# Kernel optimization log

Measured on AMD Instinct MI355X. Metric: run time of the kernel, lower is better.

Reference implementation:

```python
import jax, jax.numpy as jnp
import numpy as np


def setup_inputs() -> dict:
    key = jax.random.key(0)
    ks = jax.random.split(key, 6)
    B, S, D, U = 32, 2048, 1024, 1024
    scale = 1.0 / np.sqrt(D)
    return {
        "h_enc": jax.random.normal(ks[0], (B, S, D), dtype=jnp.float32),
        "h_dec": jax.random.normal(ks[1], (B, D), dtype=jnp.float32),
        "W_enc": jax.random.normal(ks[2], (D, U), dtype=jnp.float32) * scale,
        "b_enc": jnp.zeros((U,), dtype=jnp.float32),
        "W_dec": jax.random.normal(ks[3], (D, U), dtype=jnp.float32) * scale,
        "b_dec": jnp.zeros((U,), dtype=jnp.float32),
        "W_com": jax.random.normal(ks[4], (U, 1), dtype=jnp.float32) * (1.0 / np.sqrt(U)),
        "b_com": jnp.zeros((1,), dtype=jnp.float32),
    }


def reference(h_enc, h_dec, W_enc, b_enc, W_dec, b_dec, W_com, b_com):
    # h_enc: [B,S,D] -> projected enc features [B,S,U]
    enc_p = jnp.einsum("bsd,du->bsu", h_enc, W_enc) + b_enc
    # h_dec: [B,D] -> [B,1,U]
    dec_p = (h_dec @ W_dec + b_dec)[:, None, :]
    # additive score: [B,S,1]
    score = jnp.einsum("bsu,uo->bso", jnp.tanh(dec_p + enc_p), W_com) + b_com
    attn = jax.nn.softmax(score, axis=1)  # softmax over seq axis
    # NOTE: original code multiplies attn by the PROJECTED h_enc (reassigned)
    context_vec = jnp.sum(attn * enc_p, axis=1)  # [B,U]
    return (context_vec, attn)
```

## Files before the change

### kernel.cpp

```cpp
#include <hip/hip_runtime.h>
#include <math.h>
#include <stdint.h>

#define Bz 32
#define Sz 2048
#define Dz 1024
#define Uz 1024
#define Mz (Bz*Sz)

typedef __attribute__((ext_vector_type(8))) short bf16x8;
typedef __attribute__((ext_vector_type(4))) float f32x4;

__device__ __forceinline__ unsigned short f2bf(float f) {
    union { float f; uint32_t u; } v; v.f = f;
    uint32_t r = v.u + 0x7FFFu + ((v.u >> 16) & 1u);
    return (unsigned short)(r >> 16);
}

__device__ __forceinline__ float fast_tanh(float x) {
    float e = __expf(2.f * x);
    return 1.f - 2.f * __builtin_amdgcn_rcpf(e + 1.f);
}

#define GLD16(gsrc, ldst) \
    __builtin_amdgcn_global_load_lds((__attribute__((address_space(1))) void*)(void*)(gsrc), \
        (__attribute__((address_space(3))) void*)(ldst), 16, 0, 0)

#define CONV_BLOCKS 16384
#define WT_BLOCKS   256
#define DECI_BLOCKS 32
#define SINIT_BLOCKS 64

__global__ __launch_bounds__(256) void prep_kernel(
    const float* __restrict__ h_enc, unsigned short* __restrict__ hbf,
    const float* __restrict__ W_enc, unsigned short* __restrict__ wT,
    const float* __restrict__ b_dec, float* __restrict__ dec_p,
    const float* __restrict__ b_com, float* __restrict__ score)
{
    __shared__ float tile[64][65];
    const int bid = blockIdx.x;
    const int tid = threadIdx.x;
    if (bid < CONV_BLOCKS) {
        const size_t i = ((size_t)bid * 256 + tid) * 16;
#pragma unroll
        for (int h = 0; h < 2; ++h) {
            const float4 a = *(const float4*)(h_enc + i + h * 8);
            const float4 c = *(const float4*)(h_enc + i + h * 8 + 4);
            union { unsigned short s[8]; uint4 v; } o;
            o.s[0] = f2bf(a.x); o.s[1] = f2bf(a.y); o.s[2] = f2bf(a.z); o.s[3] = f2bf(a.w);
            o.s[4] = f2bf(c.x); o.s[5] = f2bf(c.y); o.s[6] = f2bf(c.z); o.s[7] = f2bf(c.w);
            *(uint4*)(hbf + i + h * 8) = o.v;
        }
    } else if (bid < CONV_BLOCKS + WT_BLOCKS) {
        const int b2 = bid - CONV_BLOCKS;
        const int c  = tid & 63;
        const int r0 = tid >> 6;
        const int u0 = (b2 & 15) * 64;
        const int d0 = (b2 >> 4) * 64;
        for (int r = r0; r < 64; r += 4)
            tile[r][c] = W_enc[(size_t)(d0 + r) * Uz + u0 + c];
        __syncthreads();
        for (int r = r0; r < 64; r += 4)
            wT[(size_t)(u0 + r) * Dz + d0 + c] = f2bf(tile[c][r]);
    } else if (bid < CONV_BLOCKS + WT_BLOCKS + DECI_BLOCKS) {
        const int b3 = bid - (CONV_BLOCKS + WT_BLOCKS);
        const int u4 = tid * 4;
        *(float4*)&dec_p[b3 * Uz + u4] = *(const float4*)&b_dec[u4];
    } else {
        const int b4 = bid - (CONV_BLOCKS + WT_BLOCKS + DECI_BLOCKS);
        const float bc = b_com[0];
        const int i4 = (b4 * 256 + tid) * 4;
        float4 v = {bc, bc, bc, bc};
        *(float4*)&score[i4] = v;
    }
}

__global__ __launch_bounds__(256) void dec_partial_kernel(
    const float* __restrict__ h_dec, const float* __restrict__ W_dec,
    float* __restrict__ dec_p)
{
    __shared__ float hs[128];
    const int b  = blockIdx.x >> 3;
    const int d0 = (blockIdx.x & 7) * 128;
    const int tid = threadIdx.x;
    const int u4 = tid * 4;
    if (tid < 128) hs[tid] = h_dec[b * Dz + d0 + tid];
    __syncthreads();
    float4 acc = {0.f, 0.f, 0.f, 0.f};
#pragma unroll 4
    for (int d = 0; d < 128; ++d) {
        const float  a = hs[d];
        const float4 w = *(const float4*)&W_dec[(size_t)(d0 + d) * Uz + u4];
        acc.x += a * w.x; acc.y += a * w.y; acc.z += a * w.z; acc.w += a * w.w;
    }
    float* o = dec_p + b * Uz + u4;
    atomicAdd(o + 0, acc.x); atomicAdd(o + 1, acc.y);
    atomicAdd(o + 2, acc.z); atomicAdd(o + 3, acc.w);
}

__global__ __launch_bounds__(256) void score_mfma_kernel(
    const unsigned short* __restrict__ hbf,
    const unsigned short* __restrict__ wT,
    const float* __restrict__ dec_p,
    const float* __restrict__ W_com,
    float* __restrict__ score)
{
    __shared__ unsigned short As[8 * 512];
    __shared__ unsigned short Bs[8 * 512];

    const int tid  = threadIdx.x;
    const int w    = tid >> 6;
    const int lane = tid & 63;
    const int ln   = lane & 15;
    const int q    = lane >> 4;
    const int wm   = w & 1;
    const int wn   = w >> 1;
    const int m0   = (blockIdx.x >> 1) * 128;
    const int uh   = blockIdx.x & 1;
    const int b    = m0 / Sz;
    const int ub   = uh * 512;

    const int g0 = 2 * w;
    const unsigned short* a_src0 = hbf + (size_t)(m0 + g0 * 16 + ln) * Dz + q * 8;
    const unsigned short* a_src1 = a_src0 + (size_t)16 * Dz;
    unsigned short* a_dst0 = As + g0 * 512;
    unsigned short* a_dst1 = a_dst0 + 512;

    float racc[4][4];
#pragma unroll
    for (int i = 0; i < 4; ++i)
#pragma unroll
        for (int r = 0; r < 4; ++r) racc[i][r] = 0.f;

    for (int u0 = 0; u0 < 512; u0 += 128) {
        f32x4 acc[4][4];
#pragma unroll
        for (int i = 0; i < 4; ++i)
#pragma unroll
            for (int j = 0; j < 4; ++j) acc[i][j] = (f32x4){0.f, 0.f, 0.f, 0.f};

        const unsigned short* b_src0 = wT + (size_t)(ub + u0 + g0 * 16 + ln) * Dz + q * 8;
        const unsigned short* b_src1 = b_src0 + (size_t)16 * Dz;
        unsigned short* b_dst0 = Bs + g0 * 512;
        unsigned short* b_dst1 = b_dst0 + 512;

        for (int k0 = 0; k0 < Dz; k0 += 32) {
            __syncthreads();
            GLD16(a_src0 + k0, a_dst0);
            GLD16(a_src1 + k0, a_dst1);
            GLD16(b_src0 + k0, b_dst0);
            GLD16(b_src1 + k0, b_dst1);
            __syncthreads();

            bf16x8 af[4], bfr[4];
#pragma unroll
            for (int i = 0; i < 4; ++i)
                af[i] = *(const bf16x8*)(As + (wm * 4 + i) * 512 + lane * 8);
#pragma unroll
            for (int j = 0; j < 4; ++j)
                bfr[j] = *(const bf16x8*)(Bs + (wn * 4 + j) * 512 + lane * 8);
#pragma unroll
            for (int i = 0; i < 4; ++i)
#pragma unroll
                for (int j = 0; j < 4; ++j)
                    acc[i][j] = __builtin_amdgcn_mfma_f32_16x16x32_bf16(
                        af[i], bfr[j], acc[i][j], 0, 0, 0);
        }

        float dpv[4], wcv[4];
#pragma unroll
        for (int j = 0; j < 4; ++j) {
            const int u = ub + u0 + (wn * 4 + j) * 16 + ln;
            dpv[j] = dec_p[b * Uz + u];
            wcv[j] = W_com[u];
        }
#pragma unroll
        for (int i = 0; i < 4; ++i)
#pragma unroll
            for (int r = 0; r < 4; ++r) {
                float v = 0.f;
#pragma unroll
                for (int j = 0; j < 4; ++j)
                    v += fast_tanh(acc[i][j][r] + dpv[j]) * wcv[j];
                racc[i][r] += v;
            }
    }

#pragma unroll
    for (int off = 1; off < 16; off <<= 1)
#pragma unroll
        for (int i = 0; i < 4; ++i)
#pragma unroll
            for (int r = 0; r < 4; ++r)
                racc[i][r] += __shfl_xor(racc[i][r], off, 64);
    if (ln == 0) {
#pragma unroll
        for (int i = 0; i < 4; ++i)
#pragma unroll
            for (int r = 0; r < 4; ++r)
                atomicAdd(&score[m0 + wm * 64 + i * 16 + q * 4 + r], racc[i][r]);
    }
}

__global__ __launch_bounds__(256) void softmax_init_kernel(
    const float* __restrict__ score, float* __restrict__ attn,
    const float* __restrict__ b_enc, float* __restrict__ out_ctx,
    float* __restrict__ wsum)
{
    __shared__ float red[256];
    const int tid = threadIdx.x;
    if (blockIdx.x >= 2 * Bz) {
        const int b3 = blockIdx.x - 2 * Bz;
        float4 z = {0.f, 0.f, 0.f, 0.f};
        *(float4*)&wsum[b3 * Dz + tid * 4] = z;
        return;
    }
    if (blockIdx.x >= Bz) {
        const int b2 = blockIdx.x - Bz;
        const int u4 = tid * 4;
        *(float4*)&out_ctx[b2 * Uz + u4] = *(const float4*)&b_enc[u4];
        return;
    }
    const int b = blockIdx.x;
    const float* srow = score + b * Sz;
    float v[8];
    float lm = -1e30f;
#pragma unroll
    for (int i = 0; i < 8; ++i) { v[i] = srow[i * 256 + tid]; lm = fmaxf(lm, v[i]); }
    red[tid] = lm; __syncthreads();
    for (int off = 128; off > 0; off >>= 1) {
        if (tid < off) red[tid] = fmaxf(red[tid], red[tid + off]);
        __syncthreads();
    }
    const float mx = red[0];
    __syncthreads();
    float ls = 0.f;
#pragma unroll
    for (int i = 0; i < 8; ++i) { v[i] = expf(v[i] - mx); ls += v[i]; }
    red[tid] = ls; __syncthreads();
    for (int off = 128; off > 0; off >>= 1) {
        if (tid < off) red[tid] += red[tid + off];
        __syncthreads();
    }
    const float inv = 1.f / red[0];
#pragma unroll
    for (int i = 0; i < 8; ++i) attn[b * Sz + i * 256 + tid] = v[i] * inv;
}

__global__ __launch_bounds__(256) void wsum_kernel(
    const float* __restrict__ h_enc, const float* __restrict__ attn,
    float* __restrict__ wsum)
{
    __shared__ float aw[64];
    const int b  = blockIdx.x >> 5;
    const int s0 = (blockIdx.x & 31) * 64;
    const int tid = threadIdx.x;
    if (tid < 64) aw[tid] = attn[b * Sz + s0 + tid];
    __syncthreads();
    float4 acc = {0.f, 0.f, 0.f, 0.f};
    const float* base = h_enc + ((size_t)b * Sz + s0) * Dz + tid * 4;
#pragma unroll 4
    for (int s = 0; s < 64; ++s) {
        const float a = aw[s];
        const float4 h = *(const float4*)(base + (size_t)s * Dz);
        acc.x += a * h.x; acc.y += a * h.y; acc.z += a * h.z; acc.w += a * h.w;
    }
    float* o = wsum + b * Dz + tid * 4;
    atomicAdd(o + 0, acc.x); atomicAdd(o + 1, acc.y);
    atomicAdd(o + 2, acc.z); atomicAdd(o + 3, acc.w);
}

__global__ __launch_bounds__(256) void ctx_partial_kernel(
    const float* __restrict__ wsum, const float* __restrict__ W_enc,
    float* __restrict__ out_ctx)
{
    __shared__ float hs[128];
    const int b  = blockIdx.x >> 3;
    const int d0 = (blockIdx.x & 7) * 128;
    const int tid = threadIdx.x;
    const int u4 = tid * 4;
    if (tid < 128) hs[tid] = wsum[b * Dz + d0 + tid];
    __syncthreads();
    float4 acc = {0.f, 0.f, 0.f, 0.f};
#pragma unroll 4
    for (int d = 0; d < 128; ++d) {
        const float  a = hs[d];
        const float4 wv = *(const float4*)&W_enc[(size_t)(d0 + d) * Uz + u4];
        acc.x += a * wv.x; acc.y += a * wv.y; acc.z += a * wv.z; acc.w += a * wv.w;
    }
    float* o = out_ctx + b * Uz + u4;
    atomicAdd(o + 0, acc.x); atomicAdd(o + 1, acc.y);
    atomicAdd(o + 2, acc.z); atomicAdd(o + 3, acc.w);
}

__global__ __launch_bounds__(256) void dec_proj_kernel(
    const float* __restrict__ h_dec, const float* __restrict__ W_dec,
    const float* __restrict__ b_dec, float* __restrict__ dec_p)
{
    __shared__ float hs[Dz];
    const int b = blockIdx.x >> 2;
    const int u = ((blockIdx.x & 3) << 8) + threadIdx.x;
    for (int d = threadIdx.x; d < Dz; d += 256) hs[d] = h_dec[b * Dz + d];
    __syncthreads();
    float acc = 0.f;
#pragma unroll 4
    for (int d = 0; d < Dz; ++d) acc += hs[d] * W_dec[d * Uz + u];
    dec_p[b * Uz + u] = acc + b_dec[u];
}

#define MT 64
#define NT 64
#define KT 64
__global__ __launch_bounds__(256) void score_kernel(
    const float* __restrict__ h_enc, const float* __restrict__ W_enc,
    const float* __restrict__ dec_p, const float* __restrict__ W_com,
    const float* __restrict__ b_com, float* __restrict__ score)
{
    __shared__ __align__(16) float As[KT][MT + 4];
    __shared__ __align__(16) float Bs[KT][NT + 4];
    __shared__ float red[MT][17];
    const int tid = threadIdx.x;
    const int tx = tid & 15;
    const int ty = tid >> 4;
    const int m0 = blockIdx.x * MT;
    const int b  = m0 / Sz;
    float s_acc = 0.f;
    for (int u0 = 0; u0 < Uz; u0 += NT) {
        float acc[4][4];
#pragma unroll
        for (int i = 0; i < 4; ++i)
#pragma unroll
            for (int j = 0; j < 4; ++j) acc[i][j] = 0.f;
        for (int k0 = 0; k0 < Dz; k0 += KT) {
            __syncthreads();
#pragma unroll
            for (int i = 0; i < 4; ++i) {
                const int row = ty + i * 16;
                const int c4  = tx * 4;
                const float4 v = *(const float4*)&h_enc[(size_t)(m0 + row) * Dz + k0 + c4];
                As[c4 + 0][row] = v.x; As[c4 + 1][row] = v.y;
                As[c4 + 2][row] = v.z; As[c4 + 3][row] = v.w;
            }
#pragma unroll
            for (int i = 0; i < 4; ++i) {
                const int row = ty + i * 16;
                *(float4*)&Bs[row][tx * 4] =
                    *(const float4*)&W_enc[(size_t)(k0 + row) * Uz + u0 + tx * 4];
            }
            __syncthreads();
#pragma unroll 8
            for (int k = 0; k < KT; ++k) {
                const float4 a = *(const float4*)&As[k][ty * 4];
                const float4 wv = *(const float4*)&Bs[k][tx * 4];
                acc[0][0] += a.x * wv.x; acc[0][1] += a.x * wv.y; acc[0][2] += a.x * wv.z; acc[0][3] += a.x * wv.w;
                acc[1][0] += a.y * wv.x; acc[1][1] += a.y * wv.y; acc[1][2] += a.y * wv.z; acc[1][3] += a.y * wv.w;
                acc[2][0] += a.z * wv.x; acc[2][1] += a.z * wv.y; acc[2][2] += a.z * wv.z; acc[2][3] += a.z * wv.w;
                acc[3][0] += a.w * wv.x; acc[3][1] += a.w * wv.y; acc[3][2] += a.w * wv.z; acc[3][3] += a.w * wv.w;
            }
        }
        const float4 dp = *(const float4*)&dec_p[b * Uz + u0 + tx * 4];
        const float4 wc = *(const float4*)&W_com[u0 + tx * 4];
#pragma unroll
        for (int i = 0; i < 4; ++i) {
            const float p = tanhf(acc[i][0] + dp.x) * wc.x + tanhf(acc[i][1] + dp.y) * wc.y
                          + tanhf(acc[i][2] + dp.z) * wc.z + tanhf(acc[i][3] + dp.w) * wc.w;
            red[ty * 4 + i][tx] = p;
        }
        __syncthreads();
        if (tid < MT) {
            float t = 0.f;
#pragma unroll
            for (int j = 0; j < 16; ++j) t += red[tid][j];
            s_acc += t;
        }
    }
    if (tid < MT) score[m0 + tid] = s_acc + b_com[0];
}

__global__ __launch_bounds__(256) void ctx_kernel(
    const float* __restrict__ wsum, const float* __restrict__ W_enc,
    const float* __restrict__ b_enc, float* __restrict__ out)
{
    __shared__ float hs[Dz];
    const int b = blockIdx.x >> 2;
    const int u = ((blockIdx.x & 3) << 8) + threadIdx.x;
    for (int d = threadIdx.x; d < Dz; d += 256) hs[d] = wsum[b * Dz + d];
    __syncthreads();
    float acc = 0.f;
#pragma unroll 4
    for (int d = 0; d < Dz; ++d) acc += hs[d] * W_enc[d * Uz + u];
    out[b * Uz + u] = acc + b_enc[u];
}

extern "C" void kernel_launch(void* const* d_in, const int* in_sizes, int n_in,
                              void* d_out, int out_size, void* d_ws, size_t ws_size,
                              hipStream_t stream)
{
    const float* h_enc = (const float*)d_in[0];
    const float* h_dec = (const float*)d_in[1];
    const float* W_enc = (const float*)d_in[2];
    const float* b_enc = (const float*)d_in[3];
    const float* W_dec = (const float*)d_in[4];
    const float* b_dec = (const float*)d_in[5];
    const float* W_com = (const float*)d_in[6];
    const float* b_com = (const float*)d_in[7];

    float* out_ctx  = (float*)d_out;
    float* out_attn = out_ctx + Bz * Uz;

    const size_t HBF_BYTES = (size_t)Mz * Dz * 2;
    const size_t WT_BYTES  = (size_t)Uz * Dz * 2;
    const size_t SMALL     = (size_t)(Bz*Uz + Bz*Sz + Bz*Dz) * 4;
    const size_t need      = HBF_BYTES + WT_BYTES + SMALL;

    if (ws_size >= need) {
        char* wsb = (char*)d_ws;
        unsigned short* hbf = (unsigned short*)wsb;
        unsigned short* wT  = (unsigned short*)(wsb + HBF_BYTES);
        float* dec_p = (float*)(wsb + HBF_BYTES + WT_BYTES);
        float* score = dec_p + Bz * Uz;
        float* wsum  = score + Bz * Sz;

        prep_kernel<<<CONV_BLOCKS + WT_BLOCKS + DECI_BLOCKS + SINIT_BLOCKS, 256, 0, stream>>>(
            h_enc, hbf, W_enc, wT, b_dec, dec_p, b_com, score);
        dec_partial_kernel<<<Bz * 8, 256, 0, stream>>>(h_dec, W_dec, dec_p);
        score_mfma_kernel<<<(Mz / 128) * 2, 256, 0, stream>>>(hbf, wT, dec_p, W_com, score);
        softmax_init_kernel<<<3 * Bz, 256, 0, stream>>>(score, out_attn, b_enc, out_ctx, wsum);
        wsum_kernel<<<Bz * 32, 256, 0, stream>>>(h_enc, out_attn, wsum);
        ctx_partial_kernel<<<Bz * 8, 256, 0, stream>>>(wsum, W_enc, out_ctx);
    } else {
        float* ws    = (float*)d_ws;
        float* dec_p = ws;
        float* score = ws + Bz * Uz;
        float* wsum  = ws + Bz * Uz + Bz * Sz;

        dec_proj_kernel<<<(Bz * Uz) / 256, 256, 0, stream>>>(h_dec, W_dec, b_dec, dec_p);
        score_kernel<<<Mz / MT, 256, 0, stream>>>(h_enc, W_enc, dec_p, W_com, b_com, score);
        softmax_init_kernel<<<3 * Bz, 256, 0, stream>>>(score, out_attn, b_enc, out_ctx, wsum);
        wsum_kernel<<<Bz * 32, 256, 0, stream>>>(h_enc, out_attn, wsum);
        ctx_kernel<<<(Bz * Uz) / 256, 256, 0, stream>>>(wsum, W_enc, b_enc, out_ctx);
    }
}
```

Baseline: 760.7 us.

## Double-buffer LDS tiles in score MFMA kernel to overlap loads with compute

Splits the shared-memory A and B tiles into two buffers. The next k-slice, including the first slice of the following u0 chunk, is issued into the alternate buffer while MFMAs run on the current one. This drops one of the two barriers per k-step and is meant to hide global-to-LDS latency. It doubles LDS use per block, which may lower occupancy, and whether GLD16 is asynchronous enough to overlap depends on that macro.

```diff
diff --git a/kernel.cpp b/kernel.cpp
--- a/kernel.cpp
+++ b/kernel.cpp
@@ -105,8 +105,8 @@
     const float* __restrict__ W_com,
     float* __restrict__ score)
 {
-    __shared__ unsigned short As[8 * 512];
-    __shared__ unsigned short Bs[8 * 512];
+    __shared__ unsigned short As[2][8 * 512];
+    __shared__ unsigned short Bs[2][8 * 512];
 
     const int tid  = threadIdx.x;
     const int w    = tid >> 6;
@@ -123,8 +123,7 @@
     const int g0 = 2 * w;
     const unsigned short* a_src0 = hbf + (size_t)(m0 + g0 * 16 + ln) * Dz + q * 8;
     const unsigned short* a_src1 = a_src0 + (size_t)16 * Dz;
-    unsigned short* a_dst0 = As + g0 * 512;
-    unsigned short* a_dst1 = a_dst0 + 512;
+    const unsigned short* b_base = wT + (size_t)(ub + g0 * 16 + ln) * Dz + q * 8;
 
     float racc[4][4];
 #pragma unroll
@@ -132,39 +131,77 @@
 #pragma unroll
         for (int r = 0; r < 4; ++r) racc[i][r] = 0.f;
 
+    {
+        unsigned short* a_d = &As[0][g0 * 512];
+        unsigned short* b_d = &Bs[0][g0 * 512];
+        GLD16(a_src0, a_d);
+        GLD16(a_src1, a_d + 512);
+        GLD16(b_base, b_d);
+        GLD16(b_base + (size_t)16 * Dz, b_d + 512);
+    }
+    __syncthreads();
+
+    int cur = 0;
     for (int u0 = 0; u0 < 512; u0 += 128) {
+        const unsigned short* b_src0 = b_base + (size_t)u0 * Dz;
+        const unsigned short* b_src1 = b_src0 + (size_t)16 * Dz;
+
         f32x4 acc[4][4];
 #pragma unroll
         for (int i = 0; i < 4; ++i)
 #pragma unroll
             for (int j = 0; j < 4; ++j) acc[i][j] = (f32x4){0.f, 0.f, 0.f, 0.f};
 
-        const unsigned short* b_src0 = wT + (size_t)(ub + u0 + g0 * 16 + ln) * Dz + q * 8;
-        const unsigned short* b_src1 = b_src0 + (size_t)16 * Dz;
-        unsigned short* b_dst0 = Bs + g0 * 512;
-        unsigned short* b_dst1 = b_dst0 + 512;
-
-        for (int k0 = 0; k0 < Dz; k0 += 32) {
-            __syncthreads();
-            GLD16(a_src0 + k0, a_dst0);
-            GLD16(a_src1 + k0, a_dst1);
-            GLD16(b_src0 + k0, b_dst0);
-            GLD16(b_src1 + k0, b_dst1);
-            __syncthreads();
+        for (int k0 = 0; k0 < Dz - 32; k0 += 32) {
+            unsigned short* a_d = &As[cur ^ 1][g0 * 512];
+            unsigned short* b_d = &Bs[cur ^ 1][g0 * 512];
+            GLD16(a_src0 + k0 + 32, a_d);
+            GLD16(a_src1 + k0 + 32, a_d + 512);
+            GLD16(b_src0 + k0 + 32, b_d);
+            GLD16(b_src1 + k0 + 32, b_d + 512);
 
             bf16x8 af[4], bfr[4];
 #pragma unroll
             for (int i = 0; i < 4; ++i)
-                af[i] = *(const bf16x8*)(As + (wm * 4 + i) * 512 + lane * 8);
+                af[i] = *(const bf16x8*)(&As[cur][(wm * 4 + i) * 512 + lane * 8]);
 #pragma unroll
             for (int j = 0; j < 4; ++j)
-                bfr[j] = *(const bf16x8*)(Bs + (wn * 4 + j) * 512 + lane * 8);
+                bfr[j] = *(const bf16x8*)(&Bs[cur][(wn * 4 + j) * 512 + lane * 8]);
 #pragma unroll
             for (int i = 0; i < 4; ++i)
 #pragma unroll
                 for (int j = 0; j < 4; ++j)
                     acc[i][j] = __builtin_amdgcn_mfma_f32_16x16x32_bf16(
                         af[i], bfr[j], acc[i][j], 0, 0, 0);
+            __syncthreads();
+            cur ^= 1;
+        }
+
+        {
+            if (u0 < 384) {
+                const unsigned short* nb0 = b_src0 + (size_t)128 * Dz;
+                unsigned short* a_d = &As[cur ^ 1][g0 * 512];
+                unsigned short* b_d = &Bs[cur ^ 1][g0 * 512];
+                GLD16(a_src0, a_d);
+                GLD16(a_src1, a_d + 512);
+                GLD16(nb0, b_d);
+                GLD16(nb0 + (size_t)16 * Dz, b_d + 512);
+            }
+            bf16x8 af[4], bfr[4];
+#pragma unroll
+            for (int i = 0; i < 4; ++i)
+                af[i] = *(const bf16x8*)(&As[cur][(wm * 4 + i) * 512 + lane * 8]);
+#pragma unroll
+            for (int j = 0; j < 4; ++j)
+                bfr[j] = *(const bf16x8*)(&Bs[cur][(wn * 4 + j) * 512 + lane * 8]);
+#pragma unroll
+            for (int i = 0; i < 4; ++i)
+#pragma unroll
+                for (int j = 0; j < 4; ++j)
+                    acc[i][j] = __builtin_amdgcn_mfma_f32_16x16x32_bf16(
+                        af[i], bfr[j], acc[i][j], 0, 0, 0);
+            __syncthreads();
+            cur ^= 1;
         }
 
         float dpv[4], wcv[4];
```

New measurement: 783.5 us. +3.0%, slower.
